# Optimization experiments

Hardware: AMD Instinct MI355X
Metric: run time of the kernel (lower is better)

## Reference

```python
import jax, jax.numpy as jnp
import numpy as np

B, D, K = 512, 128, 131072
TEMP = 0.07
PTR = 0  # queue_ptr starts at 0; B <= K so single contiguous write


def _normalize(x, axis):
    return x / jnp.linalg.norm(x, axis=axis, keepdims=True)


def setup_inputs() -> dict:
    key = jax.random.key(0)
    k = jax.random.split(key, 7)
    return {
        "predict0": jax.random.normal(k[0], (B, D), jnp.float32),
        "predict1": jax.random.normal(k[1], (B, D), jnp.float32),
        "project0": jax.random.normal(k[2], (B, D), jnp.float32),
        "project1": jax.random.normal(k[3], (B, D), jnp.float32),
        "queue": jax.random.normal(k[4], (D, K), jnp.float32),
        "queue_id": jax.random.randint(k[5], (K,), 0, 100000, jnp.int64) if jax.config.jax_enable_x64 else jax.random.randint(k[5], (K,), 0, 100000, jnp.int32),
        "ids": jax.random.randint(k[6], (B,), 0, 100000, jnp.int64) if jax.config.jax_enable_x64 else jax.random.randint(k[6], (B,), 0, 100000, jnp.int32),
    }


def _find_nn(proj, queue_n, queue_id, ids):
    # [B, K] similarity, mask out entries with same sample id, argmax, gather cols
    sim = proj @ queue_n                                   # [B, K]
    is_own = queue_id[None, :] == ids[:, None]             # [B, K]
    sim = jnp.where(is_own, jnp.float32(-1.0), sim)
    idx = jnp.argmax(sim, axis=1)                          # [B]
    return queue_n[:, idx]                                 # [D, B]


def _nnclr_loss(predicted, nn, temperature):
    # logits[i, j] = nn_i . predicted_j / T ; labels = arange(B)
    logits = (nn.T @ predicted.T) / temperature            # [B, B]
    logp = jax.nn.log_softmax(logits, axis=-1)
    return -jnp.mean(jnp.diagonal(logp))


def reference(predict0, predict1, project0, project1, queue, queue_id, ids):
    # forward_encoder's normalization (encoder itself is external and modeled out)
    p0 = _normalize(predict0, 1)
    p1 = _normalize(predict1, 1)
    z0 = _normalize(project0, 1)
    z1 = _normalize(project1, 1)
    queue_n = _normalize(queue, 0)  # queue stored normalized along dim 0

    # find_nn / queue are no_grad in the original
    nn0 = jax.lax.stop_gradient(_find_nn(jax.lax.stop_gradient(z0), queue_n, queue_id, ids))
    nn1 = jax.lax.stop_gradient(_find_nn(jax.lax.stop_gradient(z1), queue_n, queue_id, ids))

    loss0 = _nnclr_loss(p0, nn1, TEMP)
    loss1 = _nnclr_loss(p1, nn0, TEMP)
    loss = (loss0 + loss1) * 0.5

    # _dequeue_and_enqueue: ptr=0, B <= K -> contiguous slice write
    new_queue = jax.lax.dynamic_update_slice(queue_n, jax.lax.stop_gradient(z0.T), (0, PTR))
    new_queue_id = jax.lax.dynamic_update_slice(queue_id, ids, (PTR,))
    new_ptr = jnp.array((PTR + B) % K, dtype=queue_id.dtype)
    return loss, new_queue, new_queue_id, new_ptr
```

## Files before the change

### kernel.cpp

```cpp
#include <hip/hip_runtime.h>
#include <hip/hip_bf16.h>

typedef _Float16 half8 __attribute__((ext_vector_type(8)));
typedef _Float16 half4 __attribute__((ext_vector_type(4)));
typedef float f32x4 __attribute__((ext_vector_type(4)));

#define B 512
#define D 128
#define K 131072
#define TEMP 0.07f
#define NKB 512
#define KT_PER 16

#define INVN_OFF 0
#define Z0_OFF   131072
#define Z1_OFF   196608
#define P0_OFF   262144
#define P1_OFF   327680
#define ZF16_OFF 393216
#define QA_OFF   458752
#define PVAL_OFF 8847360
#define WKB_OFF  9371648
#define WVAL_OFF 9372672
#define IDX_OFF  9373696
#define LP_OFF   9374720

__device__ __forceinline__ void gload_lds16(const _Float16* g, _Float16* l) {
  __builtin_amdgcn_global_load_lds(
      (const __attribute__((address_space(1))) unsigned int*)g,
      (__attribute__((address_space(3))) unsigned int*)l, 16, 0, 0);
}

__global__ __launch_bounds__(128) void rownorm_k(
    const float* __restrict__ p0, const float* __restrict__ p1,
    const float* __restrict__ z0, const float* __restrict__ z1,
    float* __restrict__ w, _Float16* __restrict__ zf16) {
  int row = blockIdx.x & (B - 1);
  int which = blockIdx.x >> 9;
  const float* src; float* dst;
  switch (which) {
    case 0: src = z0; dst = w + Z0_OFF; break;
    case 1: src = z1; dst = w + Z1_OFF; break;
    case 2: src = p0; dst = w + P0_OFF; break;
    default: src = p1; dst = w + P1_OFF; break;
  }
  int tid = threadIdx.x;
  float v = src[row * D + tid];
  float s = v * v;
  #pragma unroll
  for (int o = 32; o; o >>= 1) s += __shfl_xor(s, o);
  __shared__ float sm[2];
  if ((tid & 63) == 0) sm[tid >> 6] = s;
  __syncthreads();
  float inv = rsqrtf(sm[0] + sm[1]);
  float nv = v * inv;
  dst[row * D + tid] = nv;
  if (which < 2) zf16[(which * B + row) * D + tid] = (_Float16)nv;
}

__global__ __launch_bounds__(256) void colq_k(
    const float* __restrict__ q, const int* __restrict__ qid,
    const int* __restrict__ ids, const float* __restrict__ w_z0,
    float* __restrict__ invn, float* __restrict__ out,
    _Float16* __restrict__ qA) {
  __shared__ float psum[8][128];
  __shared__ float invs[128];
  __shared__ _Float16 tile[128][136];
  int tid = threadIdx.x;
  int kb = blockIdx.x;
  int k0 = kb * 128;
  int kc = tid & 31, dg = tid >> 5;
  {
    float4 acc = {0.f, 0.f, 0.f, 0.f};
    for (int i = 0; i < 16; i++) {
      int d = dg * 16 + i;
      float4 v = *(const float4*)(q + (size_t)d * K + k0 + kc * 4);
      acc.x = fmaf(v.x, v.x, acc.x); acc.y = fmaf(v.y, v.y, acc.y);
      acc.z = fmaf(v.z, v.z, acc.z); acc.w = fmaf(v.w, v.w, acc.w);
    }
    *(float4*)&psum[dg][kc * 4] = acc;
  }
  __syncthreads();
  if (tid < 128) {
    float s = 0.f;
    #pragma unroll
    for (int g2 = 0; g2 < 8; g2++) s += psum[g2][tid];
    float inv = rsqrtf(s);
    invs[tid] = inv;
    invn[k0 + tid] = inv;
    int kk = k0 + tid;
    out[1 + (size_t)D * K + kk] = (float)((kk < B) ? ids[kk] : qid[kk]);
  }
  __syncthreads();
  {
    bool zblk = (k0 < B);
    float4 iv = *(const float4*)&invs[kc * 4];
    for (int i = 0; i < 16; i++) {
      int d = i * 8 + dg;
      float4 v = *(const float4*)(q + (size_t)d * K + k0 + kc * 4);
      float o0 = v.x * iv.x, o1 = v.y * iv.y, o2 = v.z * iv.z, o3 = v.w * iv.w;
      half4 t = {(_Float16)o0, (_Float16)o1, (_Float16)o2, (_Float16)o3};
      *(half4*)&tile[d][kc * 4] = t;
      float* oc = out + 1 + (size_t)d * K + k0 + kc * 4;
      if (zblk) {
        int col = k0 + kc * 4;
        oc[0] = w_z0[(size_t)(col + 0) * D + d];
        oc[1] = w_z0[(size_t)(col + 1) * D + d];
        oc[2] = w_z0[(size_t)(col + 2) * D + d];
        oc[3] = w_z0[(size_t)(col + 3) * D + d];
      } else {
        oc[0] = o0; oc[1] = o1; oc[2] = o2; oc[3] = o3;
      }
    }
  }
  __syncthreads();
  {
    int dc = tid >> 6, l = tid & 63;
    int g = l >> 4, c = l & 15;
    #pragma unroll
    for (int kt = 0; kt < 8; kt++) {
      half8 f;
      #pragma unroll
      for (int i = 0; i < 8; i++) {
        int d = g * 4 + (i & 3) + ((i >> 2) << 4) + dc * 32;
        f[i] = tile[d][kt * 16 + c];
      }
      int ktg = kb * 8 + kt;
      *(half8*)(qA + (size_t)((ktg * 4 + dc) * 64 + l) * 8) = f;
    }
  }
}

#define PROCESS(AF, Q4, KTG) do { \
  _Pragma("unroll") \
  for (int nt = 0; nt < 4; nt++) { \
    f32x4 acc = {0.f, 0.f, 0.f, 0.f}; \
    _Pragma("unroll") \
    for (int dc = 0; dc < 4; dc++) \
      acc = __builtin_amdgcn_mfma_f32_16x16x32_f16(AF[dc], bf[nt][dc], acc, 0, 0, 0); \
    _Pragma("unroll") \
    for (int r = 0; r < 4; r++) { \
      int qv_ = (r == 0) ? Q4.x : (r == 1) ? Q4.y : (r == 2) ? Q4.z : Q4.w; \
      float sm_ = (qv_ == myid[nt]) ? -1.0f : acc[r]; \
      best[nt] = fmaxf(best[nt], sm_); \
    } \
  } \
} while (0)

__global__ __launch_bounds__(256) void nnsearch_k(
    const _Float16* __restrict__ qA, const _Float16* __restrict__ zf16,
    const int* __restrict__ qid, const int* __restrict__ ids,
    float* __restrict__ pval) {
  __shared__ __align__(16) _Float16 qtile[2][2048];
  __shared__ __align__(16) int qid_lds[256];
  int tid = threadIdx.x;
  int flat = blockIdx.x;
  int cls = flat & 7;
  int kb = cls * 64 + (flat >> 5);
  int rg = (flat >> 3) & 3;
  int wave = tid >> 6, lane = tid & 63;
  int g = lane >> 4, c = lane & 15;
  int rowbase = rg * 256 + wave * 64;
  int kt0 = kb * KT_PER;

  gload_lds16(qA + (size_t)(((kt0 + 0) * 4 + wave) * 64 + lane) * 8,
              &qtile[0][wave * 512]);
  gload_lds16(qA + (size_t)(((kt0 + 1) * 4 + wave) * 64 + lane) * 8,
              &qtile[1][wave * 512]);
  qid_lds[tid] = qid[kb * 256 + tid];

  half8 bf[4][4];
  int myid[4];
  #pragma unroll
  for (int nt = 0; nt < 4; nt++) {
    int row = rowbase + nt * 16 + c;
    myid[nt] = ids[row & (B - 1)];
    #pragma unroll
    for (int dc = 0; dc < 4; dc++) {
      const _Float16* zr = zf16 + row * D + dc * 32 + g * 4;
      half4 lo = *(const half4*)zr;
      half4 hi = *(const half4*)(zr + 16);
      half8 f = {lo[0], lo[1], lo[2], lo[3], hi[0], hi[1], hi[2], hi[3]};
      bf[nt][dc] = f;
    }
  }
  __syncthreads();

  float best[4] = {-2.f, -2.f, -2.f, -2.f};
  for (int kt = 0; kt < KT_PER; kt++) {
    int cur = kt & 1;
    half8 af[4];
    #pragma unroll
    for (int dc = 0; dc < 4; dc++)
      af[dc] = *(const half8*)&qtile[cur][dc * 512 + lane * 8];
    int4 q4 = *(const int4*)&qid_lds[kt * 16 + g * 4];
    asm volatile("s_waitcnt lgkmcnt(0)" ::: "memory");
    __builtin_amdgcn_sched_barrier(0);
    __builtin_amdgcn_s_barrier();
    __builtin_amdgcn_sched_barrier(0);
    if (kt + 2 < KT_PER)
      gload_lds16(qA + (size_t)(((kt0 + kt + 2) * 4 + wave) * 64 + lane) * 8,
                  &qtile[cur][wave * 512]);
    PROCESS(af, q4, kt0 + kt);
    if (kt + 1 < KT_PER) {
      if (kt + 2 < KT_PER) asm volatile("s_waitcnt vmcnt(1)" ::: "memory");
      else                 asm volatile("s_waitcnt vmcnt(0)" ::: "memory");
      __builtin_amdgcn_sched_barrier(0);
      __builtin_amdgcn_s_barrier();
      __builtin_amdgcn_sched_barrier(0);
    }
  }

  #pragma unroll
  for (int nt = 0; nt < 4; nt++) {
    float v = best[nt];
    v = fmaxf(v, __shfl_xor(v, 16));
    v = fmaxf(v, __shfl_xor(v, 32));
    if (g == 0) {
      int row = rowbase + nt * 16 + c;
      pval[row * NKB + kb] = v;
    }
  }
}

__global__ __launch_bounds__(256) void nnreduce_k(
    const float* __restrict__ pval, int* __restrict__ wkb,
    float* __restrict__ wval) {
  int row = blockIdx.x;
  int tid = threadIdx.x;
  const float* p = pval + row * NKB;
  float a = p[tid], b = p[tid + 256];
  unsigned pa = (__float_as_uint(fmaf(a, 0.5f, 3.0f)) << 9) | (unsigned)(511 - tid);
  unsigned pb = (__float_as_uint(fmaf(b, 0.5f, 3.0f)) << 9) | (unsigned)(255 - tid);
  unsigned v = pa > pb ? pa : pb;
  #pragma unroll
  for (int o = 32; o; o >>= 1) {
    unsigned ov = __shfl_xor(v, o);
    v = v > ov ? v : ov;
  }
  __shared__ unsigned sv[4];
  if ((tid & 63) == 0) sv[tid >> 6] = v;
  __syncthreads();
  if (tid == 0) {
    #pragma unroll
    for (int wv = 1; wv < 4; wv++) v = v > sv[wv] ? v : sv[wv];
    int kb = 511 - (int)(v & 0x1FFu);
    wkb[row] = kb;
    wval[row] = pval[row * NKB + kb];
  }
}

__global__ __launch_bounds__(256) void nnfix_k(
    const _Float16* __restrict__ qA, const _Float16* __restrict__ zf16,
    const int* __restrict__ qid, const int* __restrict__ ids,
    const int* __restrict__ wkb, const float* __restrict__ wval,
    int* __restrict__ idxout) {
  int tid = threadIdx.x;
  int wave = tid >> 6, lane = tid & 63;
  int g = lane >> 4;
  int row = blockIdx.x * 4 + wave;
  int kb = wkb[row];
  float wv = wval[row];
  int myid = ids[row & (B - 1)];

  half8 bf[4];
  #pragma unroll
  for (int dc = 0; dc < 4; dc++) {
    const _Float16* zr = zf16 + row * D + dc * 32 + g * 4;
    half4 lo = *(const half4*)zr;
    half4 hi = *(const half4*)(zr + 16);
    half8 f = {lo[0], lo[1], lo[2], lo[3], hi[0], hi[1], hi[2], hi[3]};
    bf[dc] = f;
  }

  unsigned kbest = 0x7FFFFFFFu;
  int kt0 = kb * KT_PER;
  for (int kt = 0; kt < KT_PER; kt++) {
    int ktg = kt0 + kt;
    half8 af[4];
    #pragma unroll
    for (int dc = 0; dc < 4; dc++)
      af[dc] = *(const half8*)(qA + (size_t)((ktg * 4 + dc) * 64 + lane) * 8);
    int4 q4 = *(const int4*)(qid + ktg * 16 + g * 4);
    f32x4 acc = {0.f, 0.f, 0.f, 0.f};
    #pragma unroll
    for (int dc = 0; dc < 4; dc++)
      acc = __builtin_amdgcn_mfma_f32_16x16x32_f16(af[dc], bf[dc], acc, 0, 0, 0);
    #pragma unroll
    for (int r = 0; r < 4; r++) {
      int qv = (r == 0) ? q4.x : (r == 1) ? q4.y : (r == 2) ? q4.z : q4.w;
      float sm = (qv == myid) ? -1.0f : acc[r];
      if (sm == wv) {
        unsigned kk = (unsigned)(ktg * 16 + g * 4 + r);
        kbest = kbest < kk ? kbest : kk;
      }
    }
  }
  unsigned o1 = __shfl_xor(kbest, 16); kbest = kbest < o1 ? kbest : o1;
  unsigned o2 = __shfl_xor(kbest, 32); kbest = kbest < o2 ? kbest : o2;
  if (lane == 0) idxout[row] = (int)(kbest < (K - 1) ? kbest : (K - 1));
}

__global__ __launch_bounds__(256) void loss_k(
    const float* __restrict__ q, const float* __restrict__ invn,
    const int* __restrict__ idxout, const float* __restrict__ w,
    float* __restrict__ lpart) {
  int i0 = blockIdx.x * 8;
  int v = blockIdx.y;
  int tid = threadIdx.x;
  __shared__ float nns[8][D];
  __shared__ float rm[8][4], re[8][4], sdlds[8];
  #pragma unroll
  for (int ii = 0; ii < 4; ii++) {
    int i = ii * 2 + (tid >> 7);
    int d = tid & 127;
    int nnidx = idxout[(v ? 0 : B) + i0 + i];
    nns[i][d] = q[(size_t)d * K + nnidx] * invn[nnidx];
  }
  __syncthreads();
  const float* pr = w + (v ? P1_OFF : P0_OFF);
  const float* r0 = pr + tid * D;
  const float* r1 = pr + (tid + 256) * D;
  float a0[8] = {0, 0, 0, 0, 0, 0, 0, 0};
  float a1[8] = {0, 0, 0, 0, 0, 0, 0, 0};
  for (int d = 0; d < D; d += 4) {
    float4 x0 = *(const float4*)(r0 + d);
    float4 x1 = *(const float4*)(r1 + d);
    #pragma unroll
    for (int i = 0; i < 8; i++) {
      float4 n = *(const float4*)&nns[i][d];
      a0[i] = fmaf(x0.x, n.x, a0[i]); a0[i] = fmaf(x0.y, n.y, a0[i]);
      a0[i] = fmaf(x0.z, n.z, a0[i]); a0[i] = fmaf(x0.w, n.w, a0[i]);
      a1[i] = fmaf(x1.x, n.x, a1[i]); a1[i] = fmaf(x1.y, n.y, a1[i]);
      a1[i] = fmaf(x1.z, n.z, a1[i]); a1[i] = fmaf(x1.w, n.w, a1[i]);
    }
  }
  #pragma unroll
  for (int i = 0; i < 8; i++) {
    a0[i] *= (1.0f / TEMP);
    a1[i] *= (1.0f / TEMP);
  }
  #pragma unroll
  for (int i = 0; i < 8; i++) {
    int ig = i0 + i;
    if ((ig & 256) == 0) { if (tid == ig) sdlds[i] = a0[i]; }
    else { if (tid == (ig & 255)) sdlds[i] = a1[i]; }
  }
  int wv = tid >> 6;
  #pragma unroll
  for (int i = 0; i < 8; i++) {
    float m = fmaxf(a0[i], a1[i]);
    #pragma unroll
    for (int o = 32; o; o >>= 1) m = fmaxf(m, __shfl_xor(m, o));
    if ((tid & 63) == 0) rm[i][wv] = m;
  }
  __syncthreads();
  #pragma unroll
  for (int i = 0; i < 8; i++) {
    float m = fmaxf(fmaxf(rm[i][0], rm[i][1]), fmaxf(rm[i][2], rm[i][3]));
    float e = expf(a0[i] - m) + expf(a1[i] - m);
    #pragma unroll
    for (int o = 32; o; o >>= 1) e += __shfl_xor(e, o);
    if ((tid & 63) == 0) re[i][wv] = e;
  }
  __syncthreads();
  if (tid < 8) {
    int i = tid;
    float m = fmaxf(fmaxf(rm[i][0], rm[i][1]), fmaxf(rm[i][2], rm[i][3]));
    float s = re[i][0] + re[i][1] + re[i][2] + re[i][3];
    lpart[v * B + i0 + i] = sdlds[i] - m - logf(s);
  }
}

__global__ __launch_bounds__(256) void final_k(
    const float* __restrict__ lpart, float* __restrict__ out) {
  int tid = threadIdx.x;
  float s = lpart[tid] + lpart[tid + 256] + lpart[tid + 512] + lpart[tid + 768];
  #pragma unroll
  for (int o = 32; o; o >>= 1) s += __shfl_xor(s, o);
  __shared__ float sm[4];
  if ((tid & 63) == 0) sm[tid >> 6] = s;
  __syncthreads();
  if (tid == 0) {
    float total = sm[0] + sm[1] + sm[2] + sm[3];
    out[0] = -total * (1.0f / 1024.0f);
    out[1 + D * K + K] = 512.0f;
  }
}

extern "C" void kernel_launch(void* const* d_in, const int* in_sizes, int n_in,
                              void* d_out, int out_size, void* d_ws, size_t ws_size,
                              hipStream_t stream) {
  const float* p0 = (const float*)d_in[0];
  const float* p1 = (const float*)d_in[1];
  const float* z0 = (const float*)d_in[2];
  const float* z1 = (const float*)d_in[3];
  const float* q  = (const float*)d_in[4];
  const int* qid  = (const int*)d_in[5];
  const int* ids  = (const int*)d_in[6];
  float* out = (float*)d_out;
  float* w = (float*)d_ws;
  float* invn = w + INVN_OFF;
  _Float16* zf16 = (_Float16*)(w + ZF16_OFF);
  _Float16* qA   = (_Float16*)(w + QA_OFF);
  float* pval = w + PVAL_OFF;
  int* wkb    = (int*)(w + WKB_OFF);
  float* wval = w + WVAL_OFF;
  int* idxout = (int*)(w + IDX_OFF);
  float* lpart = w + LP_OFF;

  rownorm_k<<<2048, 128, 0, stream>>>(p0, p1, z0, z1, w, zf16);
  colq_k<<<K / 128, 256, 0, stream>>>(q, qid, ids, w + Z0_OFF, invn, out, qA);
  nnsearch_k<<<2048, 256, 0, stream>>>(qA, zf16, qid, ids, pval);
  nnreduce_k<<<1024, 256, 0, stream>>>(pval, wkb, wval);
  nnfix_k<<<256, 256, 0, stream>>>(qA, zf16, qid, ids, wkb, wval, idxout);
  dim3 gl(B / 8, 2);
  loss_k<<<gl, 256, 0, stream>>>(q, invn, idxout, w, lpart);
  final_k<<<1, 256, 0, stream>>>(lpart, out);
}
```

Before: 133.5 us.

## Double per-block K range in NN search with triple-buffered two-tile stages

Each nnsearch block now scans 32 k-tiles (512 queue columns) instead of 16, so the grid halves and there are half as many partial maxima for nnreduce. The main loop moves to a three-slot LDS ring, each slot holding two tiles. Each stage loads two tiles, prefetches two stages ahead, and uses one barrier per pair of tiles instead of two barriers per tile. The intent is to cut barrier and sync overhead, deepen memory prefetch and shrink the reduction. The cost is fewer resident blocks and more work per row in the fix-up pass, if that pass rescans the wider winning block.

```diff
diff --git a/kernel.cpp b/kernel.cpp
--- a/kernel.cpp
+++ b/kernel.cpp
@@ -9,8 +9,9 @@
 #define D 128
 #define K 131072
 #define TEMP 0.07f
-#define NKB 512
-#define KT_PER 16
+#define NKB 256
+#define KT_PER 32
+#define NSS 16
 
 #define INVN_OFF 0
 #define Z0_OFF   131072
@@ -131,7 +132,7 @@
   }
 }
 
-#define PROCESS(AF, Q4, KTG) do { \
+#define PROCESS(AF, Q4) do { \
   _Pragma("unroll") \
   for (int nt = 0; nt < 4; nt++) { \
     f32x4 acc = {0.f, 0.f, 0.f, 0.f}; \
@@ -151,23 +152,28 @@
     const _Float16* __restrict__ qA, const _Float16* __restrict__ zf16,
     const int* __restrict__ qid, const int* __restrict__ ids,
     float* __restrict__ pval) {
-  __shared__ __align__(16) _Float16 qtile[2][2048];
-  __shared__ __align__(16) int qid_lds[256];
+  __shared__ __align__(16) _Float16 qtile[3][2][2048];
+  __shared__ __align__(16) int qid_lds[512];
   int tid = threadIdx.x;
   int flat = blockIdx.x;
   int cls = flat & 7;
-  int kb = cls * 64 + (flat >> 5);
+  int kb = cls * 32 + (flat >> 5);
   int rg = (flat >> 3) & 3;
   int wave = tid >> 6, lane = tid & 63;
   int g = lane >> 4, c = lane & 15;
   int rowbase = rg * 256 + wave * 64;
   int kt0 = kb * KT_PER;
 
-  gload_lds16(qA + (size_t)(((kt0 + 0) * 4 + wave) * 64 + lane) * 8,
-              &qtile[0][wave * 512]);
-  gload_lds16(qA + (size_t)(((kt0 + 1) * 4 + wave) * 64 + lane) * 8,
-              &qtile[1][wave * 512]);
-  qid_lds[tid] = qid[kb * 256 + tid];
+  #pragma unroll
+  for (int j = 0; j < 2; j++)
+    gload_lds16(qA + (size_t)(((kt0 + j) * 4 + wave) * 64 + lane) * 8,
+                &qtile[0][j][wave * 512]);
+  #pragma unroll
+  for (int j = 0; j < 2; j++)
+    gload_lds16(qA + (size_t)(((kt0 + 2 + j) * 4 + wave) * 64 + lane) * 8,
+                &qtile[1][j][wave * 512]);
+  qid_lds[tid] = qid[kb * 512 + tid];
+  qid_lds[tid + 256] = qid[kb * 512 + tid + 256];
 
   half8 bf[4][4];
   int myid[4];
@@ -187,28 +193,35 @@
   __syncthreads();
 
   float best[4] = {-2.f, -2.f, -2.f, -2.f};
-  for (int kt = 0; kt < KT_PER; kt++) {
-    int cur = kt & 1;
-    half8 af[4];
+  int cur = 0;
+  for (int s = 0; s < NSS; s++) {
+    half8 af0[4], af1[4];
     #pragma unroll
     for (int dc = 0; dc < 4; dc++)
-      af[dc] = *(const half8*)&qtile[cur][dc * 512 + lane * 8];
-    int4 q4 = *(const int4*)&qid_lds[kt * 16 + g * 4];
-    asm volatile("s_waitcnt lgkmcnt(0)" ::: "memory");
-    __builtin_amdgcn_sched_barrier(0);
-    __builtin_amdgcn_s_barrier();
-    __builtin_amdgcn_sched_barrier(0);
-    if (kt + 2 < KT_PER)
-      gload_lds16(qA + (size_t)(((kt0 + kt + 2) * 4 + wave) * 64 + lane) * 8,
-                  &qtile[cur][wave * 512]);
-    PROCESS(af, q4, kt0 + kt);
-    if (kt + 1 < KT_PER) {
-      if (kt + 2 < KT_PER) asm volatile("s_waitcnt vmcnt(1)" ::: "memory");
-      else                 asm volatile("s_waitcnt vmcnt(0)" ::: "memory");
+      af0[dc] = *(const half8*)&qtile[cur][0][dc * 512 + lane * 8];
+    #pragma unroll
+    for (int dc = 0; dc < 4; dc++)
+      af1[dc] = *(const half8*)&qtile[cur][1][dc * 512 + lane * 8];
+    int4 q4a = *(const int4*)&qid_lds[(s * 2 + 0) * 16 + g * 4];
+    int4 q4b = *(const int4*)&qid_lds[(s * 2 + 1) * 16 + g * 4];
+    if (s + 2 < NSS) {
+      int nbuf = cur + 2; if (nbuf >= 3) nbuf -= 3;
+      #pragma unroll
+      for (int j = 0; j < 2; j++)
+        gload_lds16(qA + (size_t)(((kt0 + (s + 2) * 2 + j) * 4 + wave) * 64 + lane) * 8,
+                    &qtile[nbuf][j][wave * 512]);
+    }
+    PROCESS(af0, q4a);
+    PROCESS(af1, q4b);
+    if (s < NSS - 1) {
+      asm volatile("s_waitcnt lgkmcnt(0)" ::: "memory");
+      if (s + 2 < NSS) asm volatile("s_waitcnt vmcnt(2)" ::: "memory");
+      else             asm volatile("s_waitcnt vmcnt(0)" ::: "memory");
       __builtin_amdgcn_sched_barrier(0);
       __builtin_amdgcn_s_barrier();
       __builtin_amdgcn_sched_barrier(0);
     }
+    cur += 1; if (cur >= 3) cur -= 3;
   }
 
   #pragma unroll
@@ -229,10 +242,8 @@
   int row = blockIdx.x;
   int tid = threadIdx.x;
   const float* p = pval + row * NKB;
-  float a = p[tid], b = p[tid + 256];
-  unsigned pa = (__float_as_uint(fmaf(a, 0.5f, 3.0f)) << 9) | (unsigned)(511 - tid);
-  unsigned pb = (__float_as_uint(fmaf(b, 0.5f, 3.0f)) << 9) | (unsigned)(255 - tid);
-  unsigned v = pa > pb ? pa : pb;
+  float a = p[tid];
+  unsigned v = (__float_as_uint(fmaf(a, 0.5f, 3.0f)) << 9) | (unsigned)(NKB - 1 - tid);
   #pragma unroll
   for (int o = 32; o; o >>= 1) {
     unsigned ov = __shfl_xor(v, o);
@@ -244,7 +255,7 @@
   if (tid == 0) {
     #pragma unroll
     for (int wv = 1; wv < 4; wv++) v = v > sv[wv] ? v : sv[wv];
-    int kb = 511 - (int)(v & 0x1FFu);
+    int kb = (NKB - 1) - (int)(v & 0x1FFu);
     wkb[row] = kb;
     wval[row] = pval[row * NKB + kb];
   }
@@ -411,7 +422,7 @@
 
   rownorm_k<<<2048, 128, 0, stream>>>(p0, p1, z0, z1, w, zf16);
   colq_k<<<K / 128, 256, 0, stream>>>(q, qid, ids, w + Z0_OFF, invn, out, qA);
-  nnsearch_k<<<2048, 256, 0, stream>>>(qA, zf16, qid, ids, pval);
+  nnsearch_k<<<1024, 256, 0, stream>>>(qA, zf16, qid, ids, pval);
   nnreduce_k<<<1024, 256, 0, stream>>>(pval, wkb, wval);
   nnfix_k<<<256, 256, 0, stream>>>(qA, zf16, qid, ids, wkb, wval, idxout);
   dim3 gl(B / 8, 2);
```

After: 127.5 us. 1.05x faster.
